# Performance work log

Hardware: AMD Instinct MI355X
Metric: run time of the kernel (lower is better)

The kernel has to match this reference:

```python
import jax, jax.numpy as jnp
import numpy as np

B, S, H, T = 32, 1024, 1024, 256
WINDOW = 2
ITERATIONS = 3


def setup_inputs() -> dict:
    key = jax.random.key(0)
    k1, k2, k3, k4, k5, k6 = jax.random.split(key, 6)
    token_feats = jax.random.normal(k1, (B, S, H), dtype=jnp.float32)
    unary_score = jax.random.normal(k2, (B, S, T), dtype=jnp.float32)
    lengths = jax.random.randint(k3, (B,), S // 2, S + 1)  # in [S/2, S]
    mask = (jnp.arange(S)[None, :] < lengths[:, None]).astype(jnp.float32)
    transitions = jax.random.normal(k4, (WINDOW, T, T), dtype=jnp.float32)
    start_transitions = jax.random.normal(k5, (WINDOW, T), dtype=jnp.float32)
    end_transitions = jax.random.normal(k6, (WINDOW, T), dtype=jnp.float32)
    return {
        "token_feats": token_feats,
        "unary_score": unary_score,
        "mask": mask,
        "transitions": transitions,
        "start_transitions": start_transitions,
        "end_transitions": end_transitions,
        "lengths": lengths,
    }


def reference(token_feats, unary_score, mask, transitions, start_transitions,
              end_transitions, lengths):
    # mask unary (and token_feats, as in original; token_feats is unused in
    # the plain-transitions second-order path)
    unary = unary_score * mask[..., None]        # [B,S,T]
    _ = token_feats * mask[..., None]
    q = unary
    batch_range = jnp.arange(q.shape[0])
    for _it in range(ITERATIONS):
        q = jax.nn.softmax(q, axis=-1)
        left_sum = jnp.zeros_like(q)
        right_sum = jnp.zeros_like(q)
        for j in range(1, WINDOW + 1):
            # message from left neighbor at distance j
            left_sum = left_sum.at[:, j:].add(
                jnp.einsum('nsa,ab->nsb', q[:, :-j], transitions[j - 1]))
            # message from right neighbor at distance j
            right_sum = right_sum.at[:, :-j].add(
                jnp.einsum('nsb,ab->nsa', q[:, j:], transitions[j - 1]))
            # end transitions scatter-add at position lengths - j
            right_sum = right_sum.at[batch_range, lengths - j].add(
                end_transitions[j - 1])
        msg = left_sum + right_sum
        # start transitions on first WINDOW positions (broadcast over batch)
        msg = msg.at[:, 0:WINDOW].add(start_transitions)
        q = unary + msg
        q = q * mask[..., None]
    return q
```

## Files before the change

### kernel.cpp

```cpp
#include <hip/hip_runtime.h>
#include <hip/hip_bf16.h>
#include <cstdint>


typedef __attribute__((ext_vector_type(4))) float f32x4;
typedef __attribute__((ext_vector_type(8))) short bf16x8;

__device__ __forceinline__ void load_lds16(const void* g, void* l) {
    __builtin_amdgcn_global_load_lds(
        (const __attribute__((address_space(1))) void*)g,
        (__attribute__((address_space(3))) void*)l, 16, 0, 0);
}

__device__ __forceinline__ void wct_one(const float* __restrict__ trans,
                                        __hip_bfloat16* __restrict__ wct, int e) {
    int n = e >> 10, k = e & 1023;
    int r = k >> 8, kk = k & 255;
    float v;
    if (r == 0)      v = trans[kk * 256 + n];
    else if (r == 1) v = trans[65536 + kk * 256 + n];
    else if (r == 2) v = trans[n * 256 + kk];
    else             v = trans[65536 + n * 256 + kk];
    wct[n * 1024 + k] = __float2bfloat16(v);
}

__device__ __forceinline__ void guard_one(__hip_bfloat16* Pa, __hip_bfloat16* Pb, int g) {
    __hip_bfloat16* P = (g & 32768) ? Pb : Pa;
    int rem = g & 32767;
    int b = rem >> 10, wr = (rem >> 8) & 3, col = rem & 255;
    int row = b * 1028 + ((wr < 2) ? wr : 1024 + wr);
    P[row * 256 + col] = __float2bfloat16(0.f);
}

__device__ __forceinline__ void softmax0_row(const float* __restrict__ unary,
                                             const int* __restrict__ lengths,
                                             __hip_bfloat16* __restrict__ Pa,
                                             int row, int lane) {
    int b = row >> 10, s = row & 1023;
    float mval = (s < lengths[b]) ? 1.f : 0.f;
    float4 x = *((const float4*)(unary + (size_t)row * 256 + lane * 4));
    x.x *= mval; x.y *= mval; x.z *= mval; x.w *= mval;
    float mx = fmaxf(fmaxf(x.x, x.y), fmaxf(x.z, x.w));
    #pragma unroll
    for (int o = 32; o; o >>= 1) mx = fmaxf(mx, __shfl_xor(mx, o));
    float ea = __expf(x.x - mx), eb = __expf(x.y - mx);
    float ec = __expf(x.z - mx), ed = __expf(x.w - mx);
    float sum = ea + eb + ec + ed;
    #pragma unroll
    for (int o = 32; o; o >>= 1) sum += __shfl_xor(sum, o);
    float inv = 1.0f / sum;
    union { ushort4 u; __hip_bfloat16 h[4]; } o4;
    o4.h[0] = __float2bfloat16(ea * inv);
    o4.h[1] = __float2bfloat16(eb * inv);
    o4.h[2] = __float2bfloat16(ec * inv);
    o4.h[3] = __float2bfloat16(ed * inv);
    *((ushort4*)(Pa + ((size_t)b * 1028 + 2 + s) * 256 + lane * 4)) = o4.u;
}

__global__ __launch_bounds__(256) void prep_softmax0(
    const float* __restrict__ unary, const float* __restrict__ trans,
    const int* __restrict__ lengths,
    __hip_bfloat16* __restrict__ Pa, __hip_bfloat16* __restrict__ Pb,
    __hip_bfloat16* __restrict__ WcT)
{
    int tid = threadIdx.x, lane = tid & 63, wid = tid >> 6;
    int blk = blockIdx.x;
    int e0 = (blk * 256 + tid) * 2;
    wct_one(trans, WcT, e0);
    wct_one(trans, WcT, e0 + 1);
    int idx = blk * 256 + tid;
    if (idx < 65536) guard_one(Pa, Pb, idx);
    for (int q = 0; q < 16; ++q)
        softmax0_row(unary, lengths, Pa, blk * 64 + wid * 16 + q, lane);
}

__global__ __launch_bounds__(512, 4) void mfvi_iter_k(
    const __hip_bfloat16* __restrict__ Pin,
    const __hip_bfloat16* __restrict__ WcT,
    const float* __restrict__ unary, const int* __restrict__ lengths,
    const float* __restrict__ startT, const float* __restrict__ endT,
    __hip_bfloat16* __restrict__ Pout, float* __restrict__ out, int final_it)
{
    __shared__ __hip_bfloat16 Ps[68 * 256];
    __shared__ __hip_bfloat16 Bs[2 * 256 * 32];
    __shared__ float redA[256];
    __shared__ float redB[256];

    int tid = threadIdx.x;
    int lane = tid & 63, w = tid >> 6;
    int cn = lane & 15, quad = lane >> 4;
    int wm = (w >> 2) * 32, wn = (w & 3) * 64;
    int nslice = w & 3;
    int tile = blockIdx.x;
    int b = tile >> 4, s0 = (tile & 15) << 6;
    int len = lengths[b];
    const char* Pbase = (const char*)(Pin + ((size_t)b * 1028 + s0) * 256);

    f32x4 acc[2][4] = {};

    #pragma unroll
    for (int t = 0; t < 5; ++t) {
        int c = t * 512 + tid;
        if (t < 4 || tid < 128) {
            int row = c >> 5, ch = c & 31;
            int gch = (ch & ~7) | ((ch ^ row) & 7);
            load_lds16(Pbase + row * 512 + gch * 16, (char*)Ps + c * 16);
        }
    }

    auto stageB = [&](int bb, int p) {
        int koff = p * 64;
        #pragma unroll
        for (int c = 0; c < 2; ++c) {
            int sl = c * 512 + tid;
            int n = sl >> 2, cs = sl & 3;
            int g = cs ^ ((n >> 1) & 3);
            load_lds16((const char*)WcT + n * 2048 + koff + g * 16,
                       (char*)Bs + bb * 16384 + sl * 16);
        }
    };

    stageB(0, 0);
    __syncthreads();

    #pragma unroll 2
    for (int p = 0; p < 32; ++p) {
        if (p < 31) stageB((p + 1) & 1, p + 1);

        int region = p >> 3;
        int delta = (region == 0) ? -1 : (region == 1) ? -2
                  : (region == 2) ?  1 : 2;
        int gcb = (p & 7) * 4 + quad;

        bf16x8 af[2], bfv[4];
        #pragma unroll
        for (int i = 0; i < 2; ++i) {
            int r = wm + (i << 4) + cn + delta + 2;
            int slot = (gcb & ~7) | ((gcb ^ r) & 7);
            af[i] = *(const bf16x8*)((const char*)Ps + r * 512 + slot * 16);
        }
        #pragma unroll
        for (int j = 0; j < 4; ++j) {
            int n = wn + (j << 4) + cn;
            int cs = quad ^ ((n >> 1) & 3);
            bfv[j] = *(const bf16x8*)((const char*)Bs + (p & 1) * 16384 + n * 64 + cs * 16);
        }
        #pragma unroll
        for (int i = 0; i < 2; ++i)
            #pragma unroll
            for (int j = 0; j < 4; ++j)
                acc[i][j] = __builtin_amdgcn_mfma_f32_16x16x32_bf16(
                    af[i], bfv[j], acc[i][j], 0, 0, 0);

        __syncthreads();
    }

    #pragma unroll
    for (int i = 0; i < 2; ++i)
        #pragma unroll
        for (int j = 0; j < 4; ++j) {
            int n = wn + (j << 4) + cn;
            #pragma unroll
            for (int r = 0; r < 4; ++r) {
                int s = s0 + wm + (i << 4) + (quad << 2) + r;
                float x = acc[i][j][r];
                if (s == 0)       x += startT[n];
                if (s == 1)       x += startT[256 + n];
                if (s == len - 1) x += endT[n];
                if (s == len - 2) x += endT[256 + n];
                long idx = ((long)((b << 10) + s)) * 256 + n;
                x += unary[idx];
                acc[i][j][r] = (s < len) ? x : 0.f;
            }
        }

    if (final_it) {
        #pragma unroll
        for (int i = 0; i < 2; ++i)
            #pragma unroll
            for (int j = 0; j < 4; ++j) {
                int n = wn + (j << 4) + cn;
                #pragma unroll
                for (int r = 0; r < 4; ++r) {
                    int s = s0 + wm + (i << 4) + (quad << 2) + r;
                    out[((long)((b << 10) + s)) * 256 + n] = acc[i][j][r];
                }
            }
        return;
    }

    #pragma unroll
    for (int i = 0; i < 2; ++i)
        #pragma unroll
        for (int r = 0; r < 4; ++r) {
            float m4 = fmaxf(fmaxf(acc[i][0][r], acc[i][1][r]),
                             fmaxf(acc[i][2][r], acc[i][3][r]));
            m4 = fmaxf(m4, __shfl_xor(m4, 1));
            m4 = fmaxf(m4, __shfl_xor(m4, 2));
            m4 = fmaxf(m4, __shfl_xor(m4, 4));
            m4 = fmaxf(m4, __shfl_xor(m4, 8));
            if (cn == 0)
                redA[(nslice << 6) + wm + (i << 4) + (quad << 2) + r] = m4;
        }
    __syncthreads();
    float M[2][4];
    #pragma unroll
    for (int i = 0; i < 2; ++i)
        #pragma unroll
        for (int r = 0; r < 4; ++r) {
            int row = wm + (i << 4) + (quad << 2) + r;
            M[i][r] = fmaxf(fmaxf(redA[row], redA[64 + row]),
                            fmaxf(redA[128 + row], redA[192 + row]));
        }
    #pragma unroll
    for (int i = 0; i < 2; ++i)
        #pragma unroll
        for (int r = 0; r < 4; ++r) {
            float s4 = 0.f;
            #pragma unroll
            for (int j = 0; j < 4; ++j) {
                float e = __expf(acc[i][j][r] - M[i][r]);
                acc[i][j][r] = e;
                s4 += e;
            }
            s4 += __shfl_xor(s4, 1);
            s4 += __shfl_xor(s4, 2);
            s4 += __shfl_xor(s4, 4);
            s4 += __shfl_xor(s4, 8);
            if (cn == 0)
                redB[(nslice << 6) + wm + (i << 4) + (quad << 2) + r] = s4;
        }
    __syncthreads();
    #pragma unroll
    for (int i = 0; i < 2; ++i)
        #pragma unroll
        for (int r = 0; r < 4; ++r) {
            int row = wm + (i << 4) + (quad << 2) + r;
            float inv = 1.0f / (redB[row] + redB[64 + row] +
                                redB[128 + row] + redB[192 + row]);
            int s = s0 + row;
            #pragma unroll
            for (int j = 0; j < 4; ++j) {
                int n = wn + (j << 4) + cn;
                Pout[((size_t)b * 1028 + 2 + s) * 256 + n] =
                    __float2bfloat16(acc[i][j][r] * inv);
            }
        }
}

extern "C" void kernel_launch(void* const* d_in, const int* in_sizes, int n_in,
                              void* d_out, int out_size, void* d_ws, size_t ws_size,
                              hipStream_t stream) {
    const float* unary  = (const float*)d_in[1];
    const float* trans  = (const float*)d_in[3];
    const float* startT = (const float*)d_in[4];
    const float* endT   = (const float*)d_in[5];
    const int*   lens   = (const int*)d_in[6];

    char* ws = (char*)d_ws;
    __hip_bfloat16* Pa  = (__hip_bfloat16*)ws;
    __hip_bfloat16* Pb  = (__hip_bfloat16*)(ws + ((size_t)32 << 20));
    __hip_bfloat16* WcT = (__hip_bfloat16*)(ws + ((size_t)64 << 20));
    float* out = (float*)d_out;

    prep_softmax0<<<dim3(512), dim3(256), 0, stream>>>(unary, trans, lens, Pa, Pb, WcT);
    mfvi_iter_k<<<dim3(512), dim3(512), 0, stream>>>(Pa, WcT, unary, lens, startT, endT, Pb, nullptr, 0);
    mfvi_iter_k<<<dim3(512), dim3(512), 0, stream>>>(Pb, WcT, unary, lens, startT, endT, Pa, nullptr, 0);
    mfvi_iter_k<<<dim3(512), dim3(512), 0, stream>>>(Pa, WcT, unary, lens, startT, endT, nullptr, out, 1);
}
```

Before: 298.1 us.

## Fuse initial softmax into first iteration and pre-tile transition weights

The first-iteration softmax of the masked unary scores moves out of the prep kernel and into the first mfvi_iter kernel, which computes it directly into shared memory with halo rows, so the bf16 P buffer is no longer written and re-read. The prep kernel now only builds the bf16 transition matrix, laid out already in the swizzled per-stage tile order, so B staging becomes a contiguous copy, and zeroes the guard rows with vector stores. The cost is that halo rows are recomputed by neighbouring tiles and the first iteration loads unary through registers instead of async LDS loads.

Result: faster. 289.9 us (-2.7%).

```diff
diff --git a/kernel.cpp b/kernel.cpp
--- a/kernel.cpp
+++ b/kernel.cpp
@@ -12,74 +12,47 @@
         (__attribute__((address_space(3))) void*)l, 16, 0, 0);
 }
 
-__device__ __forceinline__ void wct_one(const float* __restrict__ trans,
-                                        __hip_bfloat16* __restrict__ wct, int e) {
-    int n = e >> 10, k = e & 1023;
-    int r = k >> 8, kk = k & 255;
-    float v;
-    if (r == 0)      v = trans[kk * 256 + n];
-    else if (r == 1) v = trans[65536 + kk * 256 + n];
-    else if (r == 2) v = trans[n * 256 + kk];
-    else             v = trans[65536 + n * 256 + kk];
-    wct[n * 1024 + k] = __float2bfloat16(v);
-}
-
-__device__ __forceinline__ void guard_one(__hip_bfloat16* Pa, __hip_bfloat16* Pb, int g) {
-    __hip_bfloat16* P = (g & 32768) ? Pb : Pa;
-    int rem = g & 32767;
-    int b = rem >> 10, wr = (rem >> 8) & 3, col = rem & 255;
-    int row = b * 1028 + ((wr < 2) ? wr : 1024 + wr);
-    P[row * 256 + col] = __float2bfloat16(0.f);
-}
-
-__device__ __forceinline__ void softmax0_row(const float* __restrict__ unary,
-                                             const int* __restrict__ lengths,
-                                             __hip_bfloat16* __restrict__ Pa,
-                                             int row, int lane) {
-    int b = row >> 10, s = row & 1023;
-    float mval = (s < lengths[b]) ? 1.f : 0.f;
-    float4 x = *((const float4*)(unary + (size_t)row * 256 + lane * 4));
-    x.x *= mval; x.y *= mval; x.z *= mval; x.w *= mval;
-    float mx = fmaxf(fmaxf(x.x, x.y), fmaxf(x.z, x.w));
-    #pragma unroll
-    for (int o = 32; o; o >>= 1) mx = fmaxf(mx, __shfl_xor(mx, o));
-    float ea = __expf(x.x - mx), eb = __expf(x.y - mx);
-    float ec = __expf(x.z - mx), ed = __expf(x.w - mx);
-    float sum = ea + eb + ec + ed;
-    #pragma unroll
-    for (int o = 32; o; o >>= 1) sum += __shfl_xor(sum, o);
-    float inv = 1.0f / sum;
-    union { ushort4 u; __hip_bfloat16 h[4]; } o4;
-    o4.h[0] = __float2bfloat16(ea * inv);
-    o4.h[1] = __float2bfloat16(eb * inv);
-    o4.h[2] = __float2bfloat16(ec * inv);
-    o4.h[3] = __float2bfloat16(ed * inv);
-    *((ushort4*)(Pa + ((size_t)b * 1028 + 2 + s) * 256 + lane * 4)) = o4.u;
-}
-
-__global__ __launch_bounds__(256) void prep_softmax0(
-    const float* __restrict__ unary, const float* __restrict__ trans,
-    const int* __restrict__ lengths,
+__global__ __launch_bounds__(256) void prep_wct(
+    const float* __restrict__ trans,
     __hip_bfloat16* __restrict__ Pa, __hip_bfloat16* __restrict__ Pb,
-    __hip_bfloat16* __restrict__ WcT)
+    __hip_bfloat16* __restrict__ WcTt)
 {
-    int tid = threadIdx.x, lane = tid & 63, wid = tid >> 6;
-    int blk = blockIdx.x;
-    int e0 = (blk * 256 + tid) * 2;
-    wct_one(trans, WcT, e0);
-    wct_one(trans, WcT, e0 + 1);
-    int idx = blk * 256 + tid;
-    if (idx < 65536) guard_one(Pa, Pb, idx);
-    for (int q = 0; q < 16; ++q)
-        softmax0_row(unary, lengths, Pa, blk * 64 + wid * 16 + q, lane);
+    int idx = blockIdx.x * 256 + threadIdx.x;
+    if (idx < 32768) {
+        int p = idx >> 10, sl = idx & 1023;
+        int n = sl >> 2, cs = sl & 3;
+        int gk = p * 4 + (cs ^ ((n >> 1) & 3));
+        union { bf16x8 v; __hip_bfloat16 h[8]; } o;
+        #pragma unroll
+        for (int e = 0; e < 8; ++e) {
+            int k = gk * 8 + e;
+            int r = k >> 8, kk = k & 255;
+            float v;
+            if (r == 0)      v = trans[kk * 256 + n];
+            else if (r == 1) v = trans[65536 + kk * 256 + n];
+            else if (r == 2) v = trans[n * 256 + kk];
+            else             v = trans[65536 + n * 256 + kk];
+            o.h[e] = __float2bfloat16(v);
+        }
+        ((bf16x8*)WcTt)[idx] = o.v;
+    } else if (idx < 40960) {
+        int g = idx - 32768;
+        __hip_bfloat16* P = (g & 4096) ? Pb : Pa;
+        int rem = g & 4095;
+        int b = rem >> 7, wr = (rem >> 5) & 3, ch = rem & 31;
+        int row = b * 1028 + ((wr < 2) ? wr : 1024 + wr);
+        bf16x8 z = {};
+        *(bf16x8*)(P + row * 256 + ch * 8) = z;
+    }
 }
 
 __global__ __launch_bounds__(512, 4) void mfvi_iter_k(
     const __hip_bfloat16* __restrict__ Pin,
-    const __hip_bfloat16* __restrict__ WcT,
+    const __hip_bfloat16* __restrict__ WcTt,
     const float* __restrict__ unary, const int* __restrict__ lengths,
     const float* __restrict__ startT, const float* __restrict__ endT,
-    __hip_bfloat16* __restrict__ Pout, float* __restrict__ out, int final_it)
+    __hip_bfloat16* __restrict__ Pout, float* __restrict__ out,
+    int first_it, int final_it)
 {
     __shared__ __hip_bfloat16 Ps[68 * 256];
     __shared__ __hip_bfloat16 Bs[2 * 256 * 32];
@@ -94,28 +67,59 @@
     int tile = blockIdx.x;
     int b = tile >> 4, s0 = (tile & 15) << 6;
     int len = lengths[b];
-    const char* Pbase = (const char*)(Pin + ((size_t)b * 1028 + s0) * 256);
 
     f32x4 acc[2][4] = {};
 
-    #pragma unroll
-    for (int t = 0; t < 5; ++t) {
-        int c = t * 512 + tid;
-        if (t < 4 || tid < 128) {
-            int row = c >> 5, ch = c & 31;
-            int gch = (ch & ~7) | ((ch ^ row) & 7);
-            load_lds16(Pbase + row * 512 + gch * 16, (char*)Ps + c * 16);
+    if (first_it) {
+        for (int q = 0; q < 9; ++q) {
+            int r = w + q * 8;
+            if (r >= 68) break;
+            int s = s0 + r - 2;
+            int ch = lane >> 1;
+            int slot = (ch & ~7) | ((ch ^ r) & 7);
+            char* dst = (char*)Ps + r * 512 + slot * 16 + (lane & 1) * 8;
+            if (s >= 0 && s < 1024) {
+                float mval = (s < len) ? 1.f : 0.f;
+                float4 x = *((const float4*)(unary + ((size_t)((b << 10) + s)) * 256 + lane * 4));
+                x.x *= mval; x.y *= mval; x.z *= mval; x.w *= mval;
+                float mx = fmaxf(fmaxf(x.x, x.y), fmaxf(x.z, x.w));
+                #pragma unroll
+                for (int o = 32; o; o >>= 1) mx = fmaxf(mx, __shfl_xor(mx, o));
+                float ea = __expf(x.x - mx), eb = __expf(x.y - mx);
+                float ec = __expf(x.z - mx), ed = __expf(x.w - mx);
+                float sum = ea + eb + ec + ed;
+                #pragma unroll
+                for (int o = 32; o; o >>= 1) sum += __shfl_xor(sum, o);
+                float inv = 1.0f / sum;
+                union { ushort4 u; __hip_bfloat16 h[4]; } o4;
+                o4.h[0] = __float2bfloat16(ea * inv);
+                o4.h[1] = __float2bfloat16(eb * inv);
+                o4.h[2] = __float2bfloat16(ec * inv);
+                o4.h[3] = __float2bfloat16(ed * inv);
+                *((ushort4*)dst) = o4.u;
+            } else {
+                ushort4 z = {0, 0, 0, 0};
+                *((ushort4*)dst) = z;
+            }
+        }
+    } else {
+        const char* Pbase = (const char*)(Pin + ((size_t)b * 1028 + s0) * 256);
+        #pragma unroll
+        for (int t = 0; t < 5; ++t) {
+            int c = t * 512 + tid;
+            if (t < 4 || tid < 128) {
+                int row = c >> 5, ch = c & 31;
+                int gch = (ch & ~7) | ((ch ^ row) & 7);
+                load_lds16(Pbase + row * 512 + gch * 16, (char*)Ps + c * 16);
+            }
         }
     }
 
     auto stageB = [&](int bb, int p) {
-        int koff = p * 64;
         #pragma unroll
         for (int c = 0; c < 2; ++c) {
             int sl = c * 512 + tid;
-            int n = sl >> 2, cs = sl & 3;
-            int g = cs ^ ((n >> 1) & 3);
-            load_lds16((const char*)WcT + n * 2048 + koff + g * 16,
+            load_lds16((const char*)WcTt + p * 16384 + sl * 16,
                        (char*)Bs + bb * 16384 + sl * 16);
         }
     };
@@ -258,13 +262,13 @@
     const int*   lens   = (const int*)d_in[6];
 
     char* ws = (char*)d_ws;
-    __hip_bfloat16* Pa  = (__hip_bfloat16*)ws;
-    __hip_bfloat16* Pb  = (__hip_bfloat16*)(ws + ((size_t)32 << 20));
-    __hip_bfloat16* WcT = (__hip_bfloat16*)(ws + ((size_t)64 << 20));
+    __hip_bfloat16* Pa   = (__hip_bfloat16*)ws;
+    __hip_bfloat16* Pb   = (__hip_bfloat16*)(ws + ((size_t)32 << 20));
+    __hip_bfloat16* WcTt = (__hip_bfloat16*)(ws + ((size_t)64 << 20));
     float* out = (float*)d_out;
 
-    prep_softmax0<<<dim3(512), dim3(256), 0, stream>>>(unary, trans, lens, Pa, Pb, WcT);
-    mfvi_iter_k<<<dim3(512), dim3(512), 0, stream>>>(Pa, WcT, unary, lens, startT, endT, Pb, nullptr, 0);
-    mfvi_iter_k<<<dim3(512), dim3(512), 0, stream>>>(Pb, WcT, unary, lens, startT, endT, Pa, nullptr, 0);
-    mfvi_iter_k<<<dim3(512), dim3(512), 0, stream>>>(Pa, WcT, unary, lens, startT, endT, nullptr, out, 1);
-}
+    prep_wct<<<dim3(160), dim3(256), 0, stream>>>(trans, Pa, Pb, WcTt);
+    mfvi_iter_k<<<dim3(512), dim3(512), 0, stream>>>(Pa, WcTt, unary, lens, startT, endT, Pb, nullptr, 1, 0);
+    mfvi_iter_k<<<dim3(512), dim3(512), 0, stream>>>(Pb, WcTt, unary, lens, startT, endT, Pa, nullptr, 0, 0);
+    mfvi_iter_k<<<dim3(512), dim3(512), 0, stream>>>(Pa, WcTt, unary, lens, startT, endT, nullptr, out, 0, 1);
+}
```
